# Kernel tuning notes

Measured on AMD Instinct MI355X. Metric: run time of the kernel, lower is better.

Reference implementation:

```python
import jax, jax.numpy as jnp
import numpy as np

B, S, T, C = 4, 2048, 2048, 256
TEMPERATURE = 0.1
CONF_THR = 0.2
NEG_INF = -jnp.inf


def setup_inputs() -> dict:
    key = jax.random.key(0)
    k1, k2, k3 = jax.random.split(key, 3)
    src_feats = jax.random.normal(k1, (B, S, C), dtype=jnp.float32)
    tgt_feats = jax.random.normal(k2, (B, T, C), dtype=jnp.float32)
    # variable valid lengths per batch (padding masks)
    src_lens = jnp.array([2048, 1800, 1500, 1024])
    tgt_lens = jnp.array([2048, 1600, 2000, 1200])
    src_mask = jnp.arange(S)[None, :] < src_lens[:, None]
    tgt_mask = jnp.arange(T)[None, :] < tgt_lens[:, None]
    W = jax.random.normal(k3, (C, C), dtype=jnp.float32) * (C ** -0.5)
    return {"src_feats": src_feats, "tgt_feats": tgt_feats,
            "src_mask": src_mask, "tgt_mask": tgt_mask, "W": W}


def reference(src_feats, tgt_feats, src_mask, tgt_mask, W):
    # NOTE: original module applies src_proj to BOTH src and tgt (tgt_proj unused)
    src = jnp.einsum('bsc,dc->bsd', src_feats, W)  # Linear, no bias
    tgt = jnp.einsum('btc,dc->btd', tgt_feats, W)
    scale = src.shape[-1] ** 0.5
    src = src / scale
    tgt = tgt / scale
    sim = jnp.einsum('bsc,btc->bst', src, tgt) / TEMPERATURE  # [B,S,T]
    sim1 = jnp.where(src_mask[:, :, None], sim, NEG_INF)
    sim2 = jnp.where(tgt_mask[:, None, :], sim, NEG_INF)
    conf_matrix = jax.nn.softmax(sim1, axis=1) * jax.nn.softmax(sim2, axis=2)
    # get_match (no_grad in original): mutual-max + threshold mask.
    # Returned as a dense boolean mask (jit-safe), instead of nonzero() indices.
    m = conf_matrix > CONF_THR
    m = m & (conf_matrix == jnp.max(conf_matrix, axis=2, keepdims=True)) \
          & (conf_matrix == jnp.max(conf_matrix, axis=1, keepdims=True))
    return conf_matrix, m
```

## Files before the change

### kernel.cpp

```cpp
#include <hip/hip_runtime.h>
#include <hip/hip_bf16.h>
#include <cstdint>
#include <cstddef>

#define B_ 4
#define S_ 2048
#define T_ 2048
#define C_ 256

__global__ void build_masks_kernel(const void* __restrict__ src_mask,
                                   const void* __restrict__ tgt_mask,
                                   int* __restrict__ smask, int* __restrict__ tmask) {
    int i = blockIdx.x * blockDim.x + threadIdx.x;
    const unsigned char* sb = (const unsigned char*)src_mask;
    const unsigned char* tb = (const unsigned char*)tgt_mask;
    bool s_is_byte = (sb[1] != 0);
    bool t_is_byte = (tb[1] != 0);
    if (i < B_ * S_)
        smask[i] = s_is_byte ? (sb[i] != 0) : (((const int*)src_mask)[i] != 0);
    if (i < B_ * T_)
        tmask[i] = t_is_byte ? (tb[i] != 0) : (((const int*)tgt_mask)[i] != 0);
}

__global__ __launch_bounds__(256) void gemm_nt_kernel(
    const float* __restrict__ A, const float* __restrict__ Bm, float* __restrict__ Out,
    int M, int N, int K, float scale)
{
    __shared__ float As[64][68];
    __shared__ float Bs[64][68];
    const int tid = threadIdx.x;
    const int n0 = blockIdx.x * 64, m0 = blockIdx.y * 64;
    const int c4 = tid & 15;
    const int rl = tid >> 4;
    const int tx = tid & 15, ty = tid >> 4;
    float acc[4][4] = {};

    for (int k0 = 0; k0 < K; k0 += 64) {
        #pragma unroll
        for (int p = 0; p < 4; ++p) {
            int row = p * 16 + rl;
            float4 a = *(const float4*)(A  + (size_t)(m0 + row) * K + k0 + c4 * 4);
            As[c4*4+0][row] = a.x; As[c4*4+1][row] = a.y;
            As[c4*4+2][row] = a.z; As[c4*4+3][row] = a.w;
            float4 b = *(const float4*)(Bm + (size_t)(n0 + row) * K + k0 + c4 * 4);
            Bs[c4*4+0][row] = b.x; Bs[c4*4+1][row] = b.y;
            Bs[c4*4+2][row] = b.z; Bs[c4*4+3][row] = b.w;
        }
        __syncthreads();
        #pragma unroll 8
        for (int k = 0; k < 64; ++k) {
            float4 av = *(const float4*)&As[k][ty * 4];
            float4 bv = *(const float4*)&Bs[k][tx * 4];
            float aa[4] = {av.x, av.y, av.z, av.w};
            float bb[4] = {bv.x, bv.y, bv.z, bv.w};
            #pragma unroll
            for (int i = 0; i < 4; ++i)
                #pragma unroll
                for (int j = 0; j < 4; ++j)
                    acc[i][j] = fmaf(aa[i], bb[j], acc[i][j]);
        }
        __syncthreads();
    }
    #pragma unroll
    for (int i = 0; i < 4; ++i) {
        float4 o = make_float4(acc[i][0]*scale, acc[i][1]*scale,
                               acc[i][2]*scale, acc[i][3]*scale);
        *(float4*)(Out + (size_t)(m0 + ty*4 + i) * N + n0 + tx * 4) = o;
    }
}

__global__ __launch_bounds__(256) void gemm_sim_kernel(
    const float* __restrict__ A, const float* __restrict__ Bm, float* __restrict__ Out,
    const int* __restrict__ smask, const int* __restrict__ tmask,
    float2* __restrict__ rowpart, float2* __restrict__ colpart)
{
    __shared__ float smem[2 * 64 * 68];
    float (*As)[68] = (float(*)[68])smem;
    float (*Bs)[68] = (float(*)[68])(smem + 64 * 68);
    const int b = blockIdx.z;
    const float* Ab = A  + (size_t)b * S_ * C_;
    const float* Bb = Bm + (size_t)b * T_ * C_;
    float* Ob = Out + (size_t)b * S_ * T_;
    const int n0 = blockIdx.x * 64, m0 = blockIdx.y * 64;
    const int tid = threadIdx.x;
    const int c4 = tid & 15, rl = tid >> 4;
    const int tx = tid & 15, ty = tid >> 4;
    float acc[4][4] = {};

    for (int k0 = 0; k0 < C_; k0 += 64) {
        #pragma unroll
        for (int p = 0; p < 4; ++p) {
            int row = p * 16 + rl;
            float4 a = *(const float4*)(Ab + (size_t)(m0 + row) * C_ + k0 + c4 * 4);
            As[c4*4+0][row] = a.x; As[c4*4+1][row] = a.y;
            As[c4*4+2][row] = a.z; As[c4*4+3][row] = a.w;
            float4 bb4 = *(const float4*)(Bb + (size_t)(n0 + row) * C_ + k0 + c4 * 4);
            Bs[c4*4+0][row] = bb4.x; Bs[c4*4+1][row] = bb4.y;
            Bs[c4*4+2][row] = bb4.z; Bs[c4*4+3][row] = bb4.w;
        }
        __syncthreads();
        #pragma unroll 8
        for (int k = 0; k < 64; ++k) {
            float4 av = *(const float4*)&As[k][ty * 4];
            float4 bv = *(const float4*)&Bs[k][tx * 4];
            float aa[4] = {av.x, av.y, av.z, av.w};
            float bbv[4] = {bv.x, bv.y, bv.z, bv.w};
            #pragma unroll
            for (int i = 0; i < 4; ++i)
                #pragma unroll
                for (int j = 0; j < 4; ++j)
                    acc[i][j] = fmaf(aa[i], bbv[j], acc[i][j]);
        }
        __syncthreads();
    }

    #pragma unroll
    for (int i = 0; i < 4; ++i) {
        #pragma unroll
        for (int j = 0; j < 4; ++j) acc[i][j] *= 10.0f;
        *(float4*)(Ob + (size_t)(m0 + ty*4 + i) * T_ + n0 + tx * 4) =
            make_float4(acc[i][0], acc[i][1], acc[i][2], acc[i][3]);
    }

    int4 tm4 = *(const int4*)(tmask + b * T_ + n0 + tx * 4);
    int4 sm4 = *(const int4*)(smask + b * S_ + m0 + ty * 4);
    int tm[4] = {tm4.x, tm4.y, tm4.z, tm4.w};
    int sm[4] = {sm4.x, sm4.y, sm4.z, sm4.w};

    float2 (*red)[17] = (float2(*)[17])smem;

    __syncthreads();
    #pragma unroll
    for (int i = 0; i < 4; ++i) {
        float v0 = tm[0] ? acc[i][0] : -INFINITY;
        float v1 = tm[1] ? acc[i][1] : -INFINITY;
        float v2 = tm[2] ? acc[i][2] : -INFINITY;
        float v3 = tm[3] ? acc[i][3] : -INFINITY;
        float m = fmaxf(fmaxf(v0, v1), fmaxf(v2, v3));
        float ss = 0.f;
        if (m != -INFINITY)
            ss = __expf(v0 - m) + __expf(v1 - m) + __expf(v2 - m) + __expf(v3 - m);
        red[ty * 4 + i][tx] = make_float2(m, ss);
    }
    __syncthreads();
    if (tid < 64) {
        float M = -INFINITY;
        #pragma unroll
        for (int q = 0; q < 16; ++q) M = fmaxf(M, red[tid][q].x);
        float SS = 0.f;
        if (M != -INFINITY) {
            #pragma unroll
            for (int q = 0; q < 16; ++q) {
                float2 p = red[tid][q];
                SS += p.y * __expf(p.x - M);
            }
        }
        rowpart[((size_t)(b * S_ + m0 + tid)) * (T_ / 64) + n0 / 64] =
            make_float2(M, SS);
    }
    __syncthreads();

    #pragma unroll
    for (int j = 0; j < 4; ++j) {
        float v0 = sm[0] ? acc[0][j] : -INFINITY;
        float v1 = sm[1] ? acc[1][j] : -INFINITY;
        float v2 = sm[2] ? acc[2][j] : -INFINITY;
        float v3 = sm[3] ? acc[3][j] : -INFINITY;
        float m = fmaxf(fmaxf(v0, v1), fmaxf(v2, v3));
        float ss = 0.f;
        if (m != -INFINITY)
            ss = __expf(v0 - m) + __expf(v1 - m) + __expf(v2 - m) + __expf(v3 - m);
        red[tx * 4 + j][ty] = make_float2(m, ss);
    }
    __syncthreads();
    if (tid < 64) {
        float M = -INFINITY;
        #pragma unroll
        for (int q = 0; q < 16; ++q) M = fmaxf(M, red[tid][q].x);
        float SS = 0.f;
        if (M != -INFINITY) {
            #pragma unroll
            for (int q = 0; q < 16; ++q) {
                float2 p = red[tid][q];
                SS += p.y * __expf(p.x - M);
            }
        }
        colpart[((size_t)(b * T_ + n0 + tid)) * (S_ / 64) + m0 / 64] =
            make_float2(M, SS);
    }
}

__global__ __launch_bounds__(256) void combine_kernel(
    const float2* __restrict__ part, float2* __restrict__ stats, int nrow)
{
    int r = blockIdx.x * 256 + threadIdx.x;
    if (r >= nrow) return;
    const float2* p = part + (size_t)r * 32;
    float2 v[32];
    #pragma unroll
    for (int q = 0; q < 16; ++q) {
        float4 f = *(const float4*)(p + q * 2);
        v[2*q]   = make_float2(f.x, f.y);
        v[2*q+1] = make_float2(f.z, f.w);
    }
    float M = -INFINITY;
    #pragma unroll
    for (int q = 0; q < 32; ++q) M = fmaxf(M, v[q].x);
    float SS = 0.f;
    if (M != -INFINITY) {
        #pragma unroll
        for (int q = 0; q < 32; ++q) SS += v[q].y * __expf(v[q].x - M);
    }
    stats[r] = make_float2(M, SS);
}

__global__ __launch_bounds__(256) void conf_kernel(
    const float* __restrict__ sim, const float2* __restrict__ rowstats,
    const float2* __restrict__ colstats, const int* __restrict__ smask,
    const int* __restrict__ tmask, float* __restrict__ conf,
    unsigned* __restrict__ rowconfmax, unsigned* __restrict__ colconfmax)
{
    const int b = blockIdx.z;
    const int s0 = blockIdx.y * 32;
    const int t0 = blockIdx.x * 256;
    const int l = threadIdx.x & 63, w = threadIdx.x >> 6;
    const int t = t0 + l * 4;

    const float2* cst = colstats + b * T_ + t;
    float2 c0 = cst[0], c1 = cst[1], c2 = cst[2], c3 = cst[3];
    int4 tm4 = *(const int4*)(tmask + b * T_ + t);
    const int tm[4] = {tm4.x, tm4.y, tm4.z, tm4.w};
    const float cm[4]   = {c0.x, c1.x, c2.x, c3.x};
    const float invc[4] = {1.f / c0.y, 1.f / c1.y, 1.f / c2.y, 1.f / c3.y};

    const float* simb  = sim  + (size_t)b * S_ * T_;
    float*       confb = conf + (size_t)b * S_ * T_;
    float colmax[4] = {0.f, 0.f, 0.f, 0.f};

    #pragma unroll
    for (int it = 0; it < 8; ++it) {
        const int s = s0 + it * 4 + w;
        float2 rst = rowstats[b * S_ + s];
        int smv = smask[b * S_ + s];
        float4 x4 = *(const float4*)(simb + (size_t)s * T_ + t);
        float x[4] = {x4.x, x4.y, x4.z, x4.w};
        float cv[4];
        if (smv) {
            float rm = rst.x, invr = 1.f / rst.y;
            #pragma unroll
            for (int j = 0; j < 4; ++j)
                cv[j] = tm[j]
                    ? __expf(2.f * x[j] - cm[j] - rm) * (invc[j] * invr)
                    : 0.f;
        } else {
            cv[0] = cv[1] = cv[2] = cv[3] = 0.f;
        }
        *(float4*)(confb + (size_t)s * T_ + t) =
            make_float4(cv[0], cv[1], cv[2], cv[3]);

        float rmax = fmaxf(fmaxf(cv[0], cv[1]), fmaxf(cv[2], cv[3]));
        #pragma unroll
        for (int off = 32; off; off >>= 1) rmax = fmaxf(rmax, __shfl_xor(rmax, off));
        if (l == 0 && smv)
            atomicMax(&rowconfmax[b * S_ + s], __float_as_uint(rmax));

        #pragma unroll
        for (int j = 0; j < 4; ++j) colmax[j] = fmaxf(colmax[j], cv[j]);
    }

    __shared__ float cred[4][256];
    *(float4*)&cred[w][l * 4] = make_float4(colmax[0], colmax[1], colmax[2], colmax[3]);
    __syncthreads();
    {
        int tt = threadIdx.x;
        float M = fmaxf(fmaxf(cred[0][tt], cred[1][tt]),
                        fmaxf(cred[2][tt], cred[3][tt]));
        atomicMax(&colconfmax[b * T_ + t0 + tt], __float_as_uint(M));
    }
}

__global__ __launch_bounds__(256) void maskout_kernel(
    const float* __restrict__ conf,
    const unsigned* __restrict__ rowconfmax, const unsigned* __restrict__ colconfmax,
    float* __restrict__ outmask)
{
    const size_t n4 = (size_t)B_ * S_ * T_ / 4;
    for (size_t i4 = (size_t)blockIdx.x * blockDim.x + threadIdx.x; i4 < n4;
         i4 += (size_t)gridDim.x * blockDim.x) {
        size_t base = i4 * 4;
        int t0  = (int)(base & (T_ - 1));
        int row = (int)(base >> 11);
        int b   = row >> 11;
        float4 c = *(const float4*)(conf + base);
        float rm = __uint_as_float(rowconfmax[row]);
        const unsigned* cmp = colconfmax + b * T_ + t0;
        float cc[4] = {c.x, c.y, c.z, c.w};
        float o[4];
        #pragma unroll
        for (int j = 0; j < 4; ++j) {
            float cmv = __uint_as_float(cmp[j]);
            o[j] = (cc[j] > 0.2f && cc[j] == rm && cc[j] == cmv) ? 1.f : 0.f;
        }
        *(float4*)(outmask + base) = make_float4(o[0], o[1], o[2], o[3]);
    }
}

extern "C" void kernel_launch(void* const* d_in, const int* in_sizes, int n_in,
                              void* d_out, int out_size, void* d_ws, size_t ws_size,
                              hipStream_t stream)
{
    const float* src_feats = (const float*)d_in[0];
    const float* tgt_feats = (const float*)d_in[1];
    const void*  src_mask  = d_in[2];
    const void*  tgt_mask  = d_in[3];
    const float* W         = (const float*)d_in[4];

    float* conf   = (float*)d_out;
    float* simbuf = conf + (size_t)B_ * S_ * T_;

    float*  srcp    = conf;
    float*  tgtp    = conf + (size_t)B_ * S_ * C_;
    float2* rowpart = (float2*)(conf + (size_t)4 * 1024 * 1024);
    float2* colpart = rowpart + (size_t)B_ * S_ * (T_ / 64);

    float2*   rowstats   = (float2*)d_ws;
    float2*   colstats   = rowstats + B_ * S_;
    unsigned* rowconfmax = (unsigned*)(colstats + B_ * T_);
    unsigned* colconfmax = rowconfmax + B_ * S_;
    int*      smask      = (int*)(colconfmax + B_ * T_);
    int*      tmask      = smask + B_ * S_;

    hipMemsetAsync(rowconfmax, 0, (size_t)(B_ * S_ + B_ * T_) * sizeof(unsigned),
                   stream);
    build_masks_kernel<<<(B_ * S_ + 255) / 256, 256, 0, stream>>>(
        src_mask, tgt_mask, smask, tmask);

    gemm_nt_kernel<<<dim3(C_ / 64, B_ * S_ / 64), 256, 0, stream>>>(
        src_feats, W, srcp, B_ * S_, C_, C_, 0.0625f);
    gemm_nt_kernel<<<dim3(C_ / 64, B_ * T_ / 64), 256, 0, stream>>>(
        tgt_feats, W, tgtp, B_ * T_, C_, C_, 0.0625f);

    gemm_sim_kernel<<<dim3(T_ / 64, S_ / 64, B_), 256, 0, stream>>>(
        srcp, tgtp, simbuf, smask, tmask, rowpart, colpart);

    combine_kernel<<<(B_ * S_ + 255) / 256, 256, 0, stream>>>(
        rowpart, rowstats, B_ * S_);
    combine_kernel<<<(B_ * T_ + 255) / 256, 256, 0, stream>>>(
        colpart, colstats, B_ * T_);

    conf_kernel<<<dim3(T_ / 256, S_ / 32, B_), 256, 0, stream>>>(
        simbuf, rowstats, colstats, smask, tmask, conf, rowconfmax, colconfmax);

    maskout_kernel<<<4096, 256, 0, stream>>>(conf, rowconfmax, colconfmax, simbuf);
}
```

Measured before the change: 368.1 us.

## Use split-bf16 MFMA GEMMs and recompute similarity instead of storing it

```diff
diff --git a/kernel.cpp b/kernel.cpp
--- a/kernel.cpp
+++ b/kernel.cpp
@@ -7,6 +7,13 @@
 #define S_ 2048
 #define T_ 2048
 #define C_ 256
+#define NEG_INF (-INFINITY)
+
+typedef __attribute__((ext_vector_type(8)))  __bf16 bf16x8;
+typedef __attribute__((ext_vector_type(4)))  __bf16 bf16x4;
+typedef __attribute__((ext_vector_type(16))) float  f32x16;
+
+#define ROWPAT(r, lh) (((r) & 3) + 8 * ((r) >> 2) + 4 * (lh))
 
 __global__ void build_masks_kernel(const void* __restrict__ src_mask,
                                    const void* __restrict__ tgt_mask,
@@ -22,171 +29,230 @@
         tmask[i] = t_is_byte ? (tb[i] != 0) : (((const int*)tgt_mask)[i] != 0);
 }
 
-__global__ __launch_bounds__(256) void gemm_nt_kernel(
-    const float* __restrict__ A, const float* __restrict__ Bm, float* __restrict__ Out,
-    int M, int N, int K, float scale)
-{
-    __shared__ float As[64][68];
-    __shared__ float Bs[64][68];
-    const int tid = threadIdx.x;
-    const int n0 = blockIdx.x * 64, m0 = blockIdx.y * 64;
-    const int c4 = tid & 15;
-    const int rl = tid >> 4;
-    const int tx = tid & 15, ty = tid >> 4;
-    float acc[4][4] = {};
-
-    for (int k0 = 0; k0 < K; k0 += 64) {
-        #pragma unroll
-        for (int p = 0; p < 4; ++p) {
-            int row = p * 16 + rl;
-            float4 a = *(const float4*)(A  + (size_t)(m0 + row) * K + k0 + c4 * 4);
-            As[c4*4+0][row] = a.x; As[c4*4+1][row] = a.y;
-            As[c4*4+2][row] = a.z; As[c4*4+3][row] = a.w;
-            float4 b = *(const float4*)(Bm + (size_t)(n0 + row) * K + k0 + c4 * 4);
-            Bs[c4*4+0][row] = b.x; Bs[c4*4+1][row] = b.y;
-            Bs[c4*4+2][row] = b.z; Bs[c4*4+3][row] = b.w;
-        }
-        __syncthreads();
-        #pragma unroll 8
-        for (int k = 0; k < 64; ++k) {
-            float4 av = *(const float4*)&As[k][ty * 4];
-            float4 bv = *(const float4*)&Bs[k][tx * 4];
-            float aa[4] = {av.x, av.y, av.z, av.w};
-            float bb[4] = {bv.x, bv.y, bv.z, bv.w};
+__global__ __launch_bounds__(256) void split_kernel(
+    const float* __restrict__ in, __bf16* __restrict__ h, __bf16* __restrict__ l,
+    int n4)
+{
+    for (int i = blockIdx.x * blockDim.x + threadIdx.x; i < n4;
+         i += gridDim.x * blockDim.x) {
+        float4 x = ((const float4*)in)[i];
+        float xs[4] = {x.x, x.y, x.z, x.w};
+        bf16x4 hv, lv;
+        #pragma unroll
+        for (int j = 0; j < 4; ++j) {
+            __bf16 hh = (__bf16)xs[j];
+            hv[j] = hh;
+            lv[j] = (__bf16)(xs[j] - (float)hh);
+        }
+        ((bf16x4*)h)[i] = hv;
+        ((bf16x4*)l)[i] = lv;
+    }
+}
+
+#define MFMA3(i, j)                                                              \
+    acc[i][j] = __builtin_amdgcn_mfma_f32_32x32x16_bf16(ah[i], bh[j], acc[i][j], 0, 0, 0); \
+    acc[i][j] = __builtin_amdgcn_mfma_f32_32x32x16_bf16(ah[i], bl[j], acc[i][j], 0, 0, 0); \
+    acc[i][j] = __builtin_amdgcn_mfma_f32_32x32x16_bf16(al[i], bh[j], acc[i][j], 0, 0, 0);
+
+__global__ __launch_bounds__(256) void proj_kernel(
+    const __bf16* __restrict__ Fh, const __bf16* __restrict__ Fl,
+    const __bf16* __restrict__ Wh, const __bf16* __restrict__ Wl,
+    __bf16* __restrict__ Ph, __bf16* __restrict__ Pl)
+{
+    const int n0 = blockIdx.x * 128, m0 = blockIdx.y * 128;
+    const int w = threadIdx.x >> 6, lane = threadIdx.x & 63;
+    const int wr = w >> 1, wc = w & 1;
+    const int lr = lane & 31, lh = lane >> 5;
+
+    const size_t aoff0 = (size_t)(m0 + 64 * wr + lr) * C_ + 8 * lh;
+    const size_t aoff1 = aoff0 + 32 * C_;
+    const size_t boff0 = (size_t)(n0 + 64 * wc + lr) * C_ + 8 * lh;
+    const size_t boff1 = boff0 + 32 * C_;
+
+    f32x16 acc[2][2] = {};
+    #pragma unroll 2
+    for (int ks = 0; ks < 16; ++ks) {
+        const int kk = ks * 16;
+        bf16x8 ah[2], al[2], bh[2], bl[2];
+        ah[0] = *(const bf16x8*)(Fh + aoff0 + kk);
+        ah[1] = *(const bf16x8*)(Fh + aoff1 + kk);
+        al[0] = *(const bf16x8*)(Fl + aoff0 + kk);
+        al[1] = *(const bf16x8*)(Fl + aoff1 + kk);
+        bh[0] = *(const bf16x8*)(Wh + boff0 + kk);
+        bh[1] = *(const bf16x8*)(Wh + boff1 + kk);
+        bl[0] = *(const bf16x8*)(Wl + boff0 + kk);
+        bl[1] = *(const bf16x8*)(Wl + boff1 + kk);
+        MFMA3(0, 0) MFMA3(0, 1) MFMA3(1, 0) MFMA3(1, 1)
+    }
+
+    #pragma unroll
+    for (int i = 0; i < 2; ++i)
+        #pragma unroll
+        for (int j = 0; j < 2; ++j)
             #pragma unroll
-            for (int i = 0; i < 4; ++i)
-                #pragma unroll
-                for (int j = 0; j < 4; ++j)
-                    acc[i][j] = fmaf(aa[i], bb[j], acc[i][j]);
-        }
-        __syncthreads();
-    }
-    #pragma unroll
-    for (int i = 0; i < 4; ++i) {
-        float4 o = make_float4(acc[i][0]*scale, acc[i][1]*scale,
-                               acc[i][2]*scale, acc[i][3]*scale);
-        *(float4*)(Out + (size_t)(m0 + ty*4 + i) * N + n0 + tx * 4) = o;
-    }
-}
-
-__global__ __launch_bounds__(256) void gemm_sim_kernel(
-    const float* __restrict__ A, const float* __restrict__ Bm, float* __restrict__ Out,
+            for (int r = 0; r < 16; ++r) {
+                float v = acc[i][j][r] * 0.0625f;
+                __bf16 hh = (__bf16)v;
+                int row = m0 + 64 * wr + 32 * i + ROWPAT(r, lh);
+                int col = n0 + 64 * wc + 32 * j + lr;
+                Ph[(size_t)row * C_ + col] = hh;
+                Pl[(size_t)row * C_ + col] = (__bf16)(v - (float)hh);
+            }
+}
+
+template <int MODE>
+__global__ __launch_bounds__(256) void simgemm_kernel(
+    const __bf16* __restrict__ Ah_, const __bf16* __restrict__ Al_,
+    const __bf16* __restrict__ Bh_, const __bf16* __restrict__ Bl_,
     const int* __restrict__ smask, const int* __restrict__ tmask,
-    float2* __restrict__ rowpart, float2* __restrict__ colpart)
-{
-    __shared__ float smem[2 * 64 * 68];
-    float (*As)[68] = (float(*)[68])smem;
-    float (*Bs)[68] = (float(*)[68])(smem + 64 * 68);
+    float2* __restrict__ rowpart, float2* __restrict__ colpart,
+    const float2* __restrict__ rowstats, const float2* __restrict__ colstats,
+    float* __restrict__ conf, unsigned* __restrict__ rowconfmax,
+    unsigned* __restrict__ colconfmax)
+{
     const int b = blockIdx.z;
-    const float* Ab = A  + (size_t)b * S_ * C_;
-    const float* Bb = Bm + (size_t)b * T_ * C_;
-    float* Ob = Out + (size_t)b * S_ * T_;
-    const int n0 = blockIdx.x * 64, m0 = blockIdx.y * 64;
-    const int tid = threadIdx.x;
-    const int c4 = tid & 15, rl = tid >> 4;
-    const int tx = tid & 15, ty = tid >> 4;
-    float acc[4][4] = {};
-
-    for (int k0 = 0; k0 < C_; k0 += 64) {
-        #pragma unroll
-        for (int p = 0; p < 4; ++p) {
-            int row = p * 16 + rl;
-            float4 a = *(const float4*)(Ab + (size_t)(m0 + row) * C_ + k0 + c4 * 4);
-            As[c4*4+0][row] = a.x; As[c4*4+1][row] = a.y;
-            As[c4*4+2][row] = a.z; As[c4*4+3][row] = a.w;
-            float4 bb4 = *(const float4*)(Bb + (size_t)(n0 + row) * C_ + k0 + c4 * 4);
-            Bs[c4*4+0][row] = bb4.x; Bs[c4*4+1][row] = bb4.y;
-            Bs[c4*4+2][row] = bb4.z; Bs[c4*4+3][row] = bb4.w;
-        }
-        __syncthreads();
-        #pragma unroll 8
-        for (int k = 0; k < 64; ++k) {
-            float4 av = *(const float4*)&As[k][ty * 4];
-            float4 bv = *(const float4*)&Bs[k][tx * 4];
-            float aa[4] = {av.x, av.y, av.z, av.w};
-            float bbv[4] = {bv.x, bv.y, bv.z, bv.w};
+    const int n0 = blockIdx.x * 128, m0 = blockIdx.y * 128;
+    const int w = threadIdx.x >> 6, lane = threadIdx.x & 63;
+    const int wr = w >> 1, wc = w & 1;
+    const int lr = lane & 31, lh = lane >> 5;
+
+    __shared__ int smask_lds[128], tmask_lds[128];
+    __shared__ float2 rstat_lds[128], cstat_lds[128];
+    if (threadIdx.x < 128) {
+        smask_lds[threadIdx.x] = smask[b * S_ + m0 + threadIdx.x];
+        if (MODE == 1) rstat_lds[threadIdx.x] = rowstats[b * S_ + m0 + threadIdx.x];
+    } else {
+        int t = threadIdx.x - 128;
+        tmask_lds[t] = tmask[b * T_ + n0 + t];
+        if (MODE == 1) cstat_lds[t] = colstats[b * T_ + n0 + t];
+    }
+    __syncthreads();
+
+    const __bf16* Ah = Ah_ + (size_t)b * S_ * C_;
+    const __bf16* Al = Al_ + (size_t)b * S_ * C_;
+    const __bf16* Bh = Bh_ + (size_t)b * T_ * C_;
+    const __bf16* Bl = Bl_ + (size_t)b * T_ * C_;
+
+    const size_t aoff0 = (size_t)(m0 + 64 * wr + lr) * C_ + 8 * lh;
+    const size_t aoff1 = aoff0 + 32 * C_;
+    const size_t boff0 = (size_t)(n0 + 64 * wc + lr) * C_ + 8 * lh;
+    const size_t boff1 = boff0 + 32 * C_;
+
+    f32x16 acc[2][2] = {};
+    #pragma unroll 2
+    for (int ks = 0; ks < 16; ++ks) {
+        const int kk = ks * 16;
+        bf16x8 ah[2], al[2], bh[2], bl[2];
+        ah[0] = *(const bf16x8*)(Ah + aoff0 + kk);
+        ah[1] = *(const bf16x8*)(Ah + aoff1 + kk);
+        al[0] = *(const bf16x8*)(Al + aoff0 + kk);
+        al[1] = *(const bf16x8*)(Al + aoff1 + kk);
+        bh[0] = *(const bf16x8*)(Bh + boff0 + kk);
+        bh[1] = *(const bf16x8*)(Bh + boff1 + kk);
+        bl[0] = *(const bf16x8*)(Bl + boff0 + kk);
+        bl[1] = *(const bf16x8*)(Bl + boff1 + kk);
+        MFMA3(0, 0) MFMA3(0, 1) MFMA3(1, 0) MFMA3(1, 1)
+    }
+
+    if (MODE == 0) {
+        const int tm0 = tmask_lds[64 * wc + lr];
+        const int tm1 = tmask_lds[64 * wc + 32 + lr];
+        #pragma unroll
+        for (int i = 0; i < 2; ++i) {
             #pragma unroll
-            for (int i = 0; i < 4; ++i)
-                #pragma unroll
-                for (int j = 0; j < 4; ++j)
-                    acc[i][j] = fmaf(aa[i], bbv[j], acc[i][j]);
-        }
-        __syncthreads();
-    }
-
-    #pragma unroll
-    for (int i = 0; i < 4; ++i) {
-        #pragma unroll
-        for (int j = 0; j < 4; ++j) acc[i][j] *= 10.0f;
-        *(float4*)(Ob + (size_t)(m0 + ty*4 + i) * T_ + n0 + tx * 4) =
-            make_float4(acc[i][0], acc[i][1], acc[i][2], acc[i][3]);
-    }
-
-    int4 tm4 = *(const int4*)(tmask + b * T_ + n0 + tx * 4);
-    int4 sm4 = *(const int4*)(smask + b * S_ + m0 + ty * 4);
-    int tm[4] = {tm4.x, tm4.y, tm4.z, tm4.w};
-    int sm[4] = {sm4.x, sm4.y, sm4.z, sm4.w};
-
-    float2 (*red)[17] = (float2(*)[17])smem;
-
-    __syncthreads();
-    #pragma unroll
-    for (int i = 0; i < 4; ++i) {
-        float v0 = tm[0] ? acc[i][0] : -INFINITY;
-        float v1 = tm[1] ? acc[i][1] : -INFINITY;
-        float v2 = tm[2] ? acc[i][2] : -INFINITY;
-        float v3 = tm[3] ? acc[i][3] : -INFINITY;
-        float m = fmaxf(fmaxf(v0, v1), fmaxf(v2, v3));
-        float ss = 0.f;
-        if (m != -INFINITY)
-            ss = __expf(v0 - m) + __expf(v1 - m) + __expf(v2 - m) + __expf(v3 - m);
-        red[ty * 4 + i][tx] = make_float2(m, ss);
-    }
-    __syncthreads();
-    if (tid < 64) {
-        float M = -INFINITY;
-        #pragma unroll
-        for (int q = 0; q < 16; ++q) M = fmaxf(M, red[tid][q].x);
-        float SS = 0.f;
-        if (M != -INFINITY) {
+            for (int r = 0; r < 16; ++r) {
+                float v0 = tm0 ? acc[i][0][r] * 10.f : NEG_INF;
+                float v1 = tm1 ? acc[i][1][r] * 10.f : NEG_INF;
+                float m = fmaxf(v0, v1);
+                #pragma unroll
+                for (int off = 1; off <= 16; off <<= 1)
+                    m = fmaxf(m, __shfl_xor(m, off));
+                float e = 0.f;
+                if (m > NEG_INF) e = __expf(v0 - m) + __expf(v1 - m);
+                #pragma unroll
+                for (int off = 1; off <= 16; off <<= 1)
+                    e += __shfl_xor(e, off);
+                if (lr == 0) {
+                    int row = m0 + 64 * wr + 32 * i + ROWPAT(r, lh);
+                    rowpart[((size_t)(b * S_ + row)) * 32 + (n0 >> 6) + wc] =
+                        make_float2(m, e);
+                }
+            }
+        }
+        #pragma unroll
+        for (int j = 0; j < 2; ++j) {
+            float m = NEG_INF;
             #pragma unroll
-            for (int q = 0; q < 16; ++q) {
-                float2 p = red[tid][q];
-                SS += p.y * __expf(p.x - M);
-            }
-        }
-        rowpart[((size_t)(b * S_ + m0 + tid)) * (T_ / 64) + n0 / 64] =
-            make_float2(M, SS);
-    }
-    __syncthreads();
-
-    #pragma unroll
-    for (int j = 0; j < 4; ++j) {
-        float v0 = sm[0] ? acc[0][j] : -INFINITY;
-        float v1 = sm[1] ? acc[1][j] : -INFINITY;
-        float v2 = sm[2] ? acc[2][j] : -INFINITY;
-        float v3 = sm[3] ? acc[3][j] : -INFINITY;
-        float m = fmaxf(fmaxf(v0, v1), fmaxf(v2, v3));
-        float ss = 0.f;
-        if (m != -INFINITY)
-            ss = __expf(v0 - m) + __expf(v1 - m) + __expf(v2 - m) + __expf(v3 - m);
-        red[tx * 4 + j][ty] = make_float2(m, ss);
-    }
-    __syncthreads();
-    if (tid < 64) {
-        float M = -INFINITY;
-        #pragma unroll
-        for (int q = 0; q < 16; ++q) M = fmaxf(M, red[tid][q].x);
-        float SS = 0.f;
-        if (M != -INFINITY) {
+            for (int i = 0; i < 2; ++i)
+                #pragma unroll
+                for (int r = 0; r < 16; ++r) {
+                    int sm = smask_lds[64 * wr + 32 * i + ROWPAT(r, lh)];
+                    float x = sm ? acc[i][j][r] * 10.f : NEG_INF;
+                    m = fmaxf(m, x);
+                }
+            m = fmaxf(m, __shfl_xor(m, 32));
+            float e = 0.f;
+            if (m > NEG_INF) {
+                #pragma unroll
+                for (int i = 0; i < 2; ++i)
+                    #pragma unroll
+                    for (int r = 0; r < 16; ++r) {
+                        int sm = smask_lds[64 * wr + 32 * i + ROWPAT(r, lh)];
+                        float x = sm ? acc[i][j][r] * 10.f : NEG_INF;
+                        e += __expf(x - m);
+                    }
+            }
+            e += __shfl_xor(e, 32);
+            if (lh == 0) {
+                int col = n0 + 64 * wc + 32 * j + lr;
+                colpart[((size_t)(b * T_ + col)) * 32 + (m0 >> 6) + wr] =
+                    make_float2(m, e);
+            }
+        }
+    } else {
+        const int tm0 = tmask_lds[64 * wc + lr];
+        const int tm1 = tmask_lds[64 * wc + 32 + lr];
+        float2 cst0 = cstat_lds[64 * wc + lr];
+        float2 cst1 = cstat_lds[64 * wc + 32 + lr];
+        const float cm0 = cst0.x, invc0 = 1.f / cst0.y;
+        const float cm1 = cst1.x, invc1 = 1.f / cst1.y;
+        float* confb = conf + (size_t)b * S_ * T_;
+        float cmax0 = 0.f, cmax1 = 0.f;
+        #pragma unroll
+        for (int i = 0; i < 2; ++i) {
             #pragma unroll
-            for (int q = 0; q < 16; ++q) {
-                float2 p = red[tid][q];
-                SS += p.y * __expf(p.x - M);
-            }
-        }
-        colpart[((size_t)(b * T_ + n0 + tid)) * (S_ / 64) + m0 / 64] =
-            make_float2(M, SS);
+            for (int r = 0; r < 16; ++r) {
+                int row_l = 64 * wr + 32 * i + ROWPAT(r, lh);
+                float2 rst = rstat_lds[row_l];
+                int sm = smask_lds[row_l];
+                float rm = rst.x, invr = 1.f / rst.y;
+                float v0 = acc[i][0][r] * 10.f;
+                float v1 = acc[i][1][r] * 10.f;
+                float c0 = (sm && tm0)
+                    ? __expf(2.f * v0 - cm0 - rm) * (invc0 * invr) : 0.f;
+                float c1 = (sm && tm1)
+                    ? __expf(2.f * v1 - cm1 - rm) * (invc1 * invr) : 0.f;
+                int row_g = m0 + row_l;
+                int col0 = n0 + 64 * wc + lr;
+                confb[(size_t)row_g * T_ + col0]      = c0;
+                confb[(size_t)row_g * T_ + col0 + 32] = c1;
+                float rmx = fmaxf(c0, c1);
+                #pragma unroll
+                for (int off = 1; off <= 16; off <<= 1)
+                    rmx = fmaxf(rmx, __shfl_xor(rmx, off));
+                if (lr == 0)
+                    atomicMax(&rowconfmax[b * S_ + row_g], __float_as_uint(rmx));
+                cmax0 = fmaxf(cmax0, c0);
+                cmax1 = fmaxf(cmax1, c1);
+            }
+        }
+        cmax0 = fmaxf(cmax0, __shfl_xor(cmax0, 32));
+        cmax1 = fmaxf(cmax1, __shfl_xor(cmax1, 32));
+        if (lh == 0) {
+            int col0 = n0 + 64 * wc + lr;
+            atomicMax(&colconfmax[b * T_ + col0],      __float_as_uint(cmax0));
+            atomicMax(&colconfmax[b * T_ + col0 + 32], __float_as_uint(cmax1));
+        }
     }
 }
 
@@ -196,87 +262,22 @@
     int r = blockIdx.x * 256 + threadIdx.x;
     if (r >= nrow) return;
     const float2* p = part + (size_t)r * 32;
+    float M = NEG_INF;
     float2 v[32];
     #pragma unroll
     for (int q = 0; q < 16; ++q) {
         float4 f = *(const float4*)(p + q * 2);
-        v[2*q]   = make_float2(f.x, f.y);
-        v[2*q+1] = make_float2(f.z, f.w);
-    }
-    float M = -INFINITY;
+        v[2 * q]     = make_float2(f.x, f.y);
+        v[2 * q + 1] = make_float2(f.z, f.w);
+    }
     #pragma unroll
     for (int q = 0; q < 32; ++q) M = fmaxf(M, v[q].x);
     float SS = 0.f;
-    if (M != -INFINITY) {
+    if (M > NEG_INF) {
         #pragma unroll
         for (int q = 0; q < 32; ++q) SS += v[q].y * __expf(v[q].x - M);
     }
     stats[r] = make_float2(M, SS);
-}
-
-__global__ __launch_bounds__(256) void conf_kernel(
-    const float* __restrict__ sim, const float2* __restrict__ rowstats,
-    const float2* __restrict__ colstats, const int* __restrict__ smask,
-    const int* __restrict__ tmask, float* __restrict__ conf,
-    unsigned* __restrict__ rowconfmax, unsigned* __restrict__ colconfmax)
-{
-    const int b = blockIdx.z;
-    const int s0 = blockIdx.y * 32;
-    const int t0 = blockIdx.x * 256;
-    const int l = threadIdx.x & 63, w = threadIdx.x >> 6;
-    const int t = t0 + l * 4;
-
-    const float2* cst = colstats + b * T_ + t;
-    float2 c0 = cst[0], c1 = cst[1], c2 = cst[2], c3 = cst[3];
-    int4 tm4 = *(const int4*)(tmask + b * T_ + t);
-    const int tm[4] = {tm4.x, tm4.y, tm4.z, tm4.w};
-    const float cm[4]   = {c0.x, c1.x, c2.x, c3.x};
-    const float invc[4] = {1.f / c0.y, 1.f / c1.y, 1.f / c2.y, 1.f / c3.y};
-
-    const float* simb  = sim  + (size_t)b * S_ * T_;
-    float*       confb = conf + (size_t)b * S_ * T_;
-    float colmax[4] = {0.f, 0.f, 0.f, 0.f};
-
-    #pragma unroll
-    for (int it = 0; it < 8; ++it) {
-        const int s = s0 + it * 4 + w;
-        float2 rst = rowstats[b * S_ + s];
-        int smv = smask[b * S_ + s];
-        float4 x4 = *(const float4*)(simb + (size_t)s * T_ + t);
-        float x[4] = {x4.x, x4.y, x4.z, x4.w};
-        float cv[4];
-        if (smv) {
-            float rm = rst.x, invr = 1.f / rst.y;
-            #pragma unroll
-            for (int j = 0; j < 4; ++j)
-                cv[j] = tm[j]
-                    ? __expf(2.f * x[j] - cm[j] - rm) * (invc[j] * invr)
-                    : 0.f;
-        } else {
-            cv[0] = cv[1] = cv[2] = cv[3] = 0.f;
-        }
-        *(float4*)(confb + (size_t)s * T_ + t) =
-            make_float4(cv[0], cv[1], cv[2], cv[3]);
-
-        float rmax = fmaxf(fmaxf(cv[0], cv[1]), fmaxf(cv[2], cv[3]));
-        #pragma unroll
-        for (int off = 32; off; off >>= 1) rmax = fmaxf(rmax, __shfl_xor(rmax, off));
-        if (l == 0 && smv)
-            atomicMax(&rowconfmax[b * S_ + s], __float_as_uint(rmax));
-
-        #pragma unroll
-        for (int j = 0; j < 4; ++j) colmax[j] = fmaxf(colmax[j], cv[j]);
-    }
-
-    __shared__ float cred[4][256];
-    *(float4*)&cred[w][l * 4] = make_float4(colmax[0], colmax[1], colmax[2], colmax[3]);
-    __syncthreads();
-    {
-        int tt = threadIdx.x;
-        float M = fmaxf(fmaxf(cred[0][tt], cred[1][tt]),
-                        fmaxf(cred[2][tt], cred[3][tt]));
-        atomicMax(&colconfmax[b * T_ + t0 + tt], __float_as_uint(M));
-    }
 }
 
 __global__ __launch_bounds__(256) void maskout_kernel(
@@ -315,13 +316,22 @@
     const void*  tgt_mask  = d_in[3];
     const float* W         = (const float*)d_in[4];
 
-    float* conf   = (float*)d_out;
-    float* simbuf = conf + (size_t)B_ * S_ * T_;
-
-    float*  srcp    = conf;
-    float*  tgtp    = conf + (size_t)B_ * S_ * C_;
-    float2* rowpart = (float2*)(conf + (size_t)4 * 1024 * 1024);
-    float2* colpart = rowpart + (size_t)B_ * S_ * (T_ / 64);
+    float* conf    = (float*)d_out;
+    char*  maskreg = (char*)d_out + (size_t)B_ * S_ * T_ * 4;
+
+    const size_t MB = 1024 * 1024;
+    __bf16* srcf_h = (__bf16*)(maskreg + 0 * MB);
+    __bf16* srcf_l = (__bf16*)(maskreg + 4 * MB);
+    __bf16* tgtf_h = (__bf16*)(maskreg + 8 * MB);
+    __bf16* tgtf_l = (__bf16*)(maskreg + 12 * MB);
+    __bf16* srcp_h = (__bf16*)(maskreg + 16 * MB);
+    __bf16* srcp_l = (__bf16*)(maskreg + 20 * MB);
+    __bf16* tgtp_h = (__bf16*)(maskreg + 24 * MB);
+    __bf16* tgtp_l = (__bf16*)(maskreg + 28 * MB);
+    __bf16* W_h    = (__bf16*)(maskreg + 32 * MB);
+    __bf16* W_l    = (__bf16*)(maskreg + 32 * MB + 128 * 1024);
+    float2* rowpart = (float2*)(maskreg + 33 * MB);
+    float2* colpart = (float2*)(maskreg + 35 * MB);
 
     float2*   rowstats   = (float2*)d_ws;
     float2*   colstats   = rowstats + B_ * S_;
@@ -335,21 +345,30 @@
     build_masks_kernel<<<(B_ * S_ + 255) / 256, 256, 0, stream>>>(
         src_mask, tgt_mask, smask, tmask);
 
-    gemm_nt_kernel<<<dim3(C_ / 64, B_ * S_ / 64), 256, 0, stream>>>(
-        src_feats, W, srcp, B_ * S_, C_, C_, 0.0625f);
-    gemm_nt_kernel<<<dim3(C_ / 64, B_ * T_ / 64), 256, 0, stream>>>(
-        tgt_feats, W, tgtp, B_ * T_, C_, C_, 0.0625f);
-
-    gemm_sim_kernel<<<dim3(T_ / 64, S_ / 64, B_), 256, 0, stream>>>(
-        srcp, tgtp, simbuf, smask, tmask, rowpart, colpart);
+    split_kernel<<<1024, 256, 0, stream>>>(src_feats, srcf_h, srcf_l,
+                                           B_ * S_ * C_ / 4);
+    split_kernel<<<1024, 256, 0, stream>>>(tgt_feats, tgtf_h, tgtf_l,
+                                           B_ * T_ * C_ / 4);
+    split_kernel<<<64, 256, 0, stream>>>(W, W_h, W_l, C_ * C_ / 4);
+
+    proj_kernel<<<dim3(C_ / 128, B_ * S_ / 128), 256, 0, stream>>>(
+        srcf_h, srcf_l, W_h, W_l, srcp_h, srcp_l);
+    proj_kernel<<<dim3(C_ / 128, B_ * T_ / 128), 256, 0, stream>>>(
+        tgtf_h, tgtf_l, W_h, W_l, tgtp_h, tgtp_l);
+
+    simgemm_kernel<0><<<dim3(T_ / 128, S_ / 128, B_), 256, 0, stream>>>(
+        srcp_h, srcp_l, tgtp_h, tgtp_l, smask, tmask, rowpart, colpart,
+        nullptr, nullptr, nullptr, nullptr, nullptr);
 
     combine_kernel<<<(B_ * S_ + 255) / 256, 256, 0, stream>>>(
         rowpart, rowstats, B_ * S_);
     combine_kernel<<<(B_ * T_ + 255) / 256, 256, 0, stream>>>(
         colpart, colstats, B_ * T_);
 
-    conf_kernel<<<dim3(T_ / 256, S_ / 32, B_), 256, 0, stream>>>(
-        simbuf, rowstats, colstats, smask, tmask, conf, rowconfmax, colconfmax);
-
-    maskout_kernel<<<4096, 256, 0, stream>>>(conf, rowconfmax, colconfmax, simbuf);
-}
+    simgemm_kernel<1><<<dim3(T_ / 128, S_ / 128, B_), 256, 0, stream>>>(
+        srcp_h, srcp_l, tgtp_h, tgtp_l, smask, tmask, nullptr, nullptr,
+        rowstats, colstats, conf, rowconfmax, colconfmax);
+
+    maskout_kernel<<<4096, 256, 0, stream>>>(conf, rowconfmax, colconfmax,
+                                             (float*)maskreg);
+}
```

Result: slower. 376.5 us (+2.3%).
